# Performance work log

Measured on AMD Instinct MI355X. Metric: run time of the kernel, lower is better.

The kernel has to match this reference:

```python
import jax, jax.numpy as jnp
import numpy as np

LENS = 0.4
DECAY = 0.2
THRESH = 0.2
LOG_SIG_MIN, LOG_SIG_MAX = -20.0, 2.0

# Surrogate-gradient spike: forward is heaviside, backward is rectangular window |x|<lens
@jax.custom_vjp
def act_fun(x):
    return (x > 0.0).astype(x.dtype)

def _act_fwd(x):
    return act_fun(x), x

def _act_bwd(x, g):
    return (g * (jnp.abs(x) < LENS).astype(g.dtype),)

act_fun.defvjp(_act_fwd, _act_bwd)


def _xavier(k, shape):
    fan_out, fan_in = shape
    lim = float(np.sqrt(6.0 / (fan_in + fan_out)))
    return jax.random.uniform(k, shape, jnp.float32, -lim, lim)


def setup_inputs() -> dict:
    key = jax.random.key(0)
    ks = jax.random.split(key, 9)
    B, IN, H, A = 4096, 512, 2048, 32
    return {
        "state": jax.random.normal(ks[0], (B, 5, IN), jnp.float32),
        "W_lif": _xavier(ks[1], (H, IN)), "b_lif": jnp.zeros((H,), jnp.float32),
        "W11": _xavier(ks[2], (H, H)), "b11": jnp.zeros((H,), jnp.float32),
        "W12": _xavier(ks[3], (H, H)), "b12": jnp.zeros((H,), jnp.float32),
        "W21": _xavier(ks[4], (H, H)), "b21": jnp.zeros((H,), jnp.float32),
        "W22": _xavier(ks[5], (H, H)), "b22": jnp.zeros((H,), jnp.float32),
        "Wm": _xavier(ks[6], (A, H)), "bm": jnp.zeros((A,), jnp.float32),
        "Wls": _xavier(ks[7], (A, H)), "bls": jnp.zeros((A,), jnp.float32),
    }


def reference(state, W_lif, b_lif, W11, b11, W12, b12, W21, b21, W22, b22, Wm, bm, Wls, bls):
    x_seq = jnp.repeat(state, 3, axis=1)
    # precompute fc(x) for all steps in one GEMM: [B,15,H]
    fc = jnp.einsum('bti,hi->bth', x_seq, W_lif) + b_lif
    B, T, H = fc.shape

    def step(carry, fc_t):
        mem, spike = carry
        mem1 = mem * DECAY * (1.0 - spike) + fc_t
        spike1 = act_fun(mem1 - THRESH)
        return (mem1, spike1), spike1

    init = (jnp.zeros((B, H), fc.dtype), jnp.zeros((B, H), fc.dtype))
    _, spikes = jax.lax.scan(step, init, jnp.swapaxes(fc, 0, 1))  # [T,B,H]
    x = jnp.mean(spikes, axis=0)  # [B,H]

    x1 = jax.nn.relu(x @ W11.T + b11)
    x1 = jax.nn.relu(x1 @ W12.T + b12)
    mean = x1 @ Wm.T + bm

    x2 = jax.nn.relu(x @ W21.T + b21)
    x2 = jax.nn.relu(x2 @ W22.T + b22)
    log_std = jnp.clip(x2 @ Wls.T + bls, LOG_SIG_MIN, LOG_SIG_MAX)
    return mean, log_std
```

## Files before the change

### kernel.cpp

```cpp
#include <hip/hip_runtime.h>
#include <hip/hip_bf16.h>


typedef _Float16 f16;
using f32x4 = __attribute__((ext_vector_type(4))) float;
using f16x8 = __attribute__((ext_vector_type(8))) f16;

#define MFMA16(a, b, c) __builtin_amdgcn_mfma_f32_16x16x32_f16((a), (b), (c), 0, 0, 0)
#define VMW8()  asm volatile("s_waitcnt vmcnt(8)" ::: "memory")
#define VMW6()  asm volatile("s_waitcnt vmcnt(6)" ::: "memory")
#define VMW0()  asm volatile("s_waitcnt vmcnt(0)" ::: "memory")
#define LGKM0() asm volatile("s_waitcnt lgkmcnt(0)" ::: "memory")
#define BARRIER() __builtin_amdgcn_s_barrier()
#define SCHED0() __builtin_amdgcn_sched_barrier(0)

__device__ __forceinline__ void gload16(const void* g, void* l) {
  __builtin_amdgcn_global_load_lds(
      (const __attribute__((address_space(1))) unsigned int*)g,
      (__attribute__((address_space(3))) unsigned int*)l, 16, 0, 0);
}

__device__ __forceinline__ void cvt8(const float4& a, const float4& b, f16* dst) {
  f16x8 d;
  d[0] = (f16)a.x; d[1] = (f16)a.y; d[2] = (f16)a.z; d[3] = (f16)a.w;
  d[4] = (f16)b.x; d[5] = (f16)b.y; d[6] = (f16)b.z; d[7] = (f16)b.w;
  *(f16x8*)dst = d;
}

__global__ __launch_bounds__(256) void cvtall_kernel(
    const float* __restrict__ state, const float* __restrict__ wlif,
    const float* __restrict__ w11, const float* __restrict__ w21,
    const float* __restrict__ w12, const float* __restrict__ w22,
    const float* __restrict__ wm, const float* __restrict__ wls,
    f16* __restrict__ s16, f16* __restrict__ wl16, f16* __restrict__ w4,
    f16* __restrict__ wmh, f16* __restrict__ wlsh)
{
  int i = blockIdx.x * 256 + threadIdx.x;
  const float* src; f16* dst; int k, ks;
  if (i < 1310720)        { src = state; dst = s16;  k = i;           ks = k; }
  else if (i < 1441792)   { src = wlif;  dst = wl16; k = i - 1310720; ks = k; }
  else if (i < 3538944) {
    int j = i - 1441792; int w = j >> 19;
    src = (w == 0) ? w11 : (w == 1) ? w21 : (w == 2) ? w12 : w22;
    dst = w4; k = j; ks = j & 524287;
  }
  else if (i < 3547136)   { src = wm;  dst = wmh;  k = i - 3538944; ks = k; }
  else if (i < 3555328)   { src = wls; dst = wlsh; k = i - 3547136; ks = k; }
  else return;
  const float4* s4 = (const float4*)src;
  float4 a = s4[(size_t)ks * 2], b = s4[(size_t)ks * 2 + 1];
  cvt8(a, b, dst + (size_t)k * 8);
}

__global__ __launch_bounds__(512, 1) void lif256_kernel(
    const f16* __restrict__ S,
    const f16* __restrict__ W,
    const float* __restrict__ bl,
    f16* __restrict__ X)
{
  __shared__ alignas(16) f16 lds[73728];

  const int tid = threadIdx.x, wid = tid >> 6, lane = tid & 63;
  const int wg = ((int)blockIdx.x % 8) * 32 + (int)blockIdx.x / 8;
  const int bn = wg & 15, bm = wg >> 4;
  const int b0 = bm * 256, h0 = bn * 128;
  const int wr0 = (wid >> 1) * 64, wc0 = (wid & 1) * 64;
  const int fr = lane & 15, fq = lane >> 4;
  const int sr = tid >> 3, scb = (tid & 7) * 16;

  f32x4 acc[4][4] = {};
  float mem[4][4][4] = {};
  unsigned pcnt[4][4] = {};

  char* Lb = (char*)&lds[0];
  const int xsw = (fr & 7) << 4;
  const int x0 = (fq * 16) ^ xsw;
  const int x1 = (64 + fq * 16) ^ xsw;
  char* const pA0 = Lb + (wr0 + fr) * 128 + x0;
  char* const pA1 = Lb + (wr0 + fr) * 128 + x1;
  char* const pB0 = Lb + 98304 + (wc0 + fr) * 128 + x0;
  char* const pB1 = Lb + 98304 + (wc0 + fr) * 128 + x1;

  const f16* sBase[4]; const f16* wBase[2];
#pragma unroll
  for (int l = 0; l < 4; ++l) {
    const int row = l * 64 + sr;
    const int c2 = scb ^ ((row & 7) << 4);
    sBase[l] = S + (size_t)(b0 + row) * 2560 + (c2 >> 1);
  }
#pragma unroll
  for (int l = 0; l < 2; ++l) {
    const int row = l * 64 + sr;
    const int c2 = scb ^ ((row & 7) << 4);
    wBase[l] = W + (size_t)(h0 + row) * 512 + (c2 >> 1);
  }

  auto STAGE = [&](int soA, int soB, int g) {
    const int koff = (g >> 3) * 512 + (g & 7) * 64;
    const int kw = (g & 7) * 64;
#pragma unroll
    for (int l = 0; l < 4; ++l)
      gload16(sBase[l] + koff, Lb + soA + l * 8192 + tid * 16);
#pragma unroll
    for (int l = 0; l < 2; ++l)
      gload16(wBase[l] + kw, Lb + 98304 + soB + l * 8192 + tid * 16);
  };

  const float bias[4] = { bl[h0 + wc0 + fr],      bl[h0 + wc0 + 16 + fr],
                          bl[h0 + wc0 + 32 + fr], bl[h0 + wc0 + 48 + fr] };

  STAGE(0, 0, 0);
  STAGE(32768, 16384, 1);
  VMW6();
  BARRIER();
  SCHED0();

  int soA = 0, soB = 0;
  int soStA = 65536, soStB = 32768;
  for (int g = 0; g < 40; ++g) {
    if (g + 2 < 40) STAGE(soStA, soStB, g + 2);
    SCHED0();

    f16x8 b[4][2], a[4][2];
#pragma unroll
    for (int nf = 0; nf < 4; ++nf) {
      b[nf][0] = *(const f16x8*)(pB0 + soB + nf * 2048);
      b[nf][1] = *(const f16x8*)(pB1 + soB + nf * 2048);
    }
#pragma unroll
    for (int mf = 0; mf < 4; ++mf) {
      a[mf][0] = *(const f16x8*)(pA0 + soA + mf * 2048);
      a[mf][1] = *(const f16x8*)(pA1 + soA + mf * 2048);
    }

    __builtin_amdgcn_s_setprio(1);
#pragma unroll
    for (int mf = 0; mf < 4; ++mf)
#pragma unroll
      for (int nf = 0; nf < 4; ++nf) {
        acc[mf][nf] = MFMA16(a[mf][0], b[nf][0], acc[mf][nf]);
        acc[mf][nf] = MFMA16(a[mf][1], b[nf][1], acc[mf][nf]);
      }
    __builtin_amdgcn_s_setprio(0);

    if ((g & 7) == 7) {
#pragma unroll
      for (int mf = 0; mf < 4; ++mf)
#pragma unroll
        for (int nf = 0; nf < 4; ++nf) {
          unsigned pc = pcnt[mf][nf];
#pragma unroll
          for (int r = 0; r < 4; ++r) {
            const float fc = acc[mf][nf][r] + bias[nf];
            float m = mem[mf][nf][r];
            const unsigned inc = 1u << (8 * r);
#pragma unroll
            for (int j = 0; j < 3; ++j) {
              m = ((m > 0.2f) ? 0.f : m * 0.2f) + fc;
              pc += (m > 0.2f) ? inc : 0u;
            }
            mem[mf][nf][r] = m;
          }
          pcnt[mf][nf] = pc;
          acc[mf][nf] = f32x4{0.f, 0.f, 0.f, 0.f};
        }
    }

    LGKM0();
    if (g + 2 < 40)      { VMW6(); }
    else if (g + 1 < 40) { VMW0(); }
    BARRIER();
    SCHED0();

    soA   = (soA   == 65536) ? 0 : soA   + 32768;
    soB   = (soB   == 32768) ? 0 : soB   + 16384;
    soStA = (soStA == 65536) ? 0 : soStA + 32768;
    soStB = (soStB == 32768) ? 0 : soStB + 16384;
  }

#pragma unroll
  for (int nf = 0; nf < 4; ++nf) {
    const int col = h0 + wc0 + nf * 16 + fr;
#pragma unroll
    for (int mf = 0; mf < 4; ++mf) {
      const int row0 = b0 + wr0 + mf * 16 + fq * 4;
#pragma unroll
      for (int r = 0; r < 4; ++r) {
        const float c = (float)((pcnt[mf][nf] >> (8 * r)) & 255u);
        X[(size_t)(row0 + r) * 2048 + col] = (f16)(c / 15.0f);
      }
    }
  }
}

__global__ __launch_bounds__(512, 2) void trunk256_kernel(
    const f16* __restrict__ A0, const f16* __restrict__ A1, int lda,
    const f16* __restrict__ W0, const f16* __restrict__ W1,
    const float* __restrict__ bb0, const float* __restrict__ bb1,
    f16* __restrict__ C0, f16* __restrict__ C1, int ldc,
    int nbm, int nbn_half, int K)
{
  __shared__ alignas(16) f16 lds[4][256 * 64];

  const int tid = threadIdx.x, wid = tid >> 6, lane = tid & 63;
  const int nwg = nbm * nbn_half * 2, q8 = nwg / 8;
  const int wg = ((int)blockIdx.x % 8) * q8 + (int)blockIdx.x / 8;
  const int bmi = wg % nbm, t = wg / nbm;
  const int half = (t >= nbn_half);
  const f16* Ap = half ? A1 : A0;
  const f16* Wp = half ? W1 : W0;
  const float* bias = half ? bb1 : bb0;
  f16* C = half ? C1 : C0;
  const int bm0 = bmi * 256;
  const int bn0 = (half ? t - nbn_half : t) * 256;

  const int wr0 = (wid >> 2) * 128, wc0 = (wid & 3) * 64;
  const int fr = lane & 15, fq = lane >> 4;
  const int sr = tid >> 3, scb = (tid & 7) * 16;

  f32x4 acc[8][4] = {};
  const int NT = K / 64;

  char* Lb = (char*)&lds[0][0];
  const int xsw = (fr & 7) << 4;
  const int x0 = (fq * 16) ^ xsw;
  const int x1 = (64 + fq * 16) ^ xsw;
  char* const pA0 = Lb + (wr0 + fr) * 128 + x0;
  char* const pA1 = Lb + (wr0 + fr) * 128 + x1;
  char* const pB0 = Lb + 65536 + (wc0 + fr) * 128 + x0;
  char* const pB1 = Lb + 65536 + (wc0 + fr) * 128 + x1;

  const f16* aBase[4]; const f16* wBase[4];
#pragma unroll
  for (int l = 0; l < 4; ++l) {
    const int row = l * 64 + sr;
    const int c2 = scb ^ ((row & 7) << 4);
    aBase[l] = Ap + (size_t)(bm0 + row) * lda + (c2 >> 1);
    wBase[l] = Wp + (size_t)(bn0 + row) * K + (c2 >> 1);
  }

  auto STAGE_A = [&](int slot, int kt) {
    const int koff = kt * 64;
#pragma unroll
    for (int l = 0; l < 4; ++l)
      gload16(aBase[l] + koff, Lb + slot * 32768 + l * 8192 + tid * 16);
  };
  auto STAGE_B = [&](int slot, int kt) {
    const int koff = kt * 64;
#pragma unroll
    for (int l = 0; l < 4; ++l)
      gload16(wBase[l] + koff, Lb + 65536 + slot * 32768 + l * 8192 + tid * 16);
  };

  STAGE_A(0, 0); STAGE_B(0, 0);
  STAGE_A(1, 1); STAGE_B(1, 1);
  VMW8();
  BARRIER();
  SCHED0();

#pragma unroll 2
  for (int kt = 0; kt < NT; ++kt) {
    const int slot = kt & 1;
    const int so = slot * 32768;

    auto QUAD = [&](int mbase, f16x8 (&b)[4][2], f16x8 (&a)[2][2]) {
      __builtin_amdgcn_s_setprio(1);
#pragma unroll
      for (int nf = 0; nf < 4; ++nf) {
        acc[mbase][nf]     = MFMA16(a[0][0], b[nf][0], acc[mbase][nf]);
        acc[mbase][nf]     = MFMA16(a[0][1], b[nf][1], acc[mbase][nf]);
        acc[mbase + 1][nf] = MFMA16(a[1][0], b[nf][0], acc[mbase + 1][nf]);
        acc[mbase + 1][nf] = MFMA16(a[1][1], b[nf][1], acc[mbase + 1][nf]);
      }
      __builtin_amdgcn_s_setprio(0);
    };

    f16x8 b[4][2], a0[2][2], a1[2][2];
#pragma unroll
    for (int nf = 0; nf < 4; ++nf) {
      b[nf][0] = *(const f16x8*)(pB0 + so + nf * 2048);
      b[nf][1] = *(const f16x8*)(pB1 + so + nf * 2048);
    }
#pragma unroll
    for (int i = 0; i < 2; ++i) {
      a0[i][0] = *(const f16x8*)(pA0 + so + i * 2048);
      a0[i][1] = *(const f16x8*)(pA1 + so + i * 2048);
    }
    LGKM0();
    BARRIER();
    if (kt + 2 < NT) STAGE_B(slot, kt + 2);
    SCHED0();

#pragma unroll
    for (int i = 0; i < 2; ++i) {
      a1[i][0] = *(const f16x8*)(pA0 + so + (2 + i) * 2048);
      a1[i][1] = *(const f16x8*)(pA1 + so + (2 + i) * 2048);
    }
    QUAD(0, b, a0);
    LGKM0(); SCHED0();
#pragma unroll
    for (int i = 0; i < 2; ++i) {
      a0[i][0] = *(const f16x8*)(pA0 + so + (4 + i) * 2048);
      a0[i][1] = *(const f16x8*)(pA1 + so + (4 + i) * 2048);
    }
    QUAD(2, b, a1);
    LGKM0(); SCHED0();
#pragma unroll
    for (int i = 0; i < 2; ++i) {
      a1[i][0] = *(const f16x8*)(pA0 + so + (6 + i) * 2048);
      a1[i][1] = *(const f16x8*)(pA1 + so + (6 + i) * 2048);
    }
    QUAD(4, b, a0);
    LGKM0();
    BARRIER();
    if (kt + 2 < NT) STAGE_A(slot, kt + 2);
    SCHED0();
    QUAD(6, b, a1);
    if (kt + 2 < NT)      { VMW8(); }
    else if (kt + 1 < NT) { VMW0(); }
    BARRIER();
    SCHED0();
  }

#pragma unroll
  for (int nf = 0; nf < 4; ++nf) {
    const int col = bn0 + wc0 + nf * 16 + fr;
    const float bv = bias[col];
#pragma unroll
    for (int m = 0; m < 8; ++m) {
      const int row0 = bm0 + wr0 + m * 16 + fq * 4;
#pragma unroll
      for (int r = 0; r < 4; ++r) {
        float v = fmaxf(acc[m][nf][r] + bv, 0.f);
        C[(size_t)(row0 + r) * ldc + col] = (f16)v;
      }
    }
  }
}

__global__ __launch_bounds__(256) void head_kernel(
    const f16* __restrict__ H1, const f16* __restrict__ H2,
    const f16* __restrict__ Wm, const float* __restrict__ bm,
    const f16* __restrict__ Wls, const float* __restrict__ bls,
    float* __restrict__ OUT, int M, int K)
{
  const int tid = threadIdx.x, wid = tid >> 6, lane = tid & 63;
  const int m0 = blockIdx.x * 64 + wid * 16;
  const int kb = (lane >> 4) * 8, fr = lane & 15, fq = lane >> 4;

  f32x4 a1[2] = {}, a2[2] = {};
  for (int k0 = 0; k0 < K; k0 += 32) {
    f16x8 f1 = *(const f16x8*)&H1[(size_t)(m0 + fr) * K + k0 + kb];
    f16x8 f2 = *(const f16x8*)&H2[(size_t)(m0 + fr) * K + k0 + kb];
#pragma unroll
    for (int n = 0; n < 2; ++n) {
      f16x8 wm = *(const f16x8*)&Wm[(size_t)(n * 16 + fr) * K + k0 + kb];
      f16x8 wl = *(const f16x8*)&Wls[(size_t)(n * 16 + fr) * K + k0 + kb];
      a1[n] = MFMA16(f1, wm, a1[n]);
      a2[n] = MFMA16(f2, wl, a2[n]);
    }
  }

#pragma unroll
  for (int n = 0; n < 2; ++n) {
    const int col = n * 16 + fr;
    const float bvm = bm[col];
    const float bvl = bls[col];
#pragma unroll
    for (int r = 0; r < 4; ++r) {
      const int row = m0 + fq * 4 + r;
      OUT[(size_t)row * 32 + col] = a1[n][r] + bvm;
      float lv = a2[n][r] + bvl;
      OUT[(size_t)M * 32 + (size_t)row * 32 + col] = fminf(fmaxf(lv, -20.f), 2.f);
    }
  }
}

extern "C" void kernel_launch(void* const* d_in, const int* in_sizes, int n_in,
                              void* d_out, int out_size, void* d_ws, size_t ws_size,
                              hipStream_t stream) {
  const float* state = (const float*)d_in[0];
  const float* W_lif = (const float*)d_in[1];
  const float* b_lif = (const float*)d_in[2];
  const float* W11   = (const float*)d_in[3];
  const float* b11   = (const float*)d_in[4];
  const float* W12   = (const float*)d_in[5];
  const float* b12   = (const float*)d_in[6];
  const float* W21   = (const float*)d_in[7];
  const float* b21   = (const float*)d_in[8];
  const float* W22   = (const float*)d_in[9];
  const float* b22   = (const float*)d_in[10];
  const float* Wm    = (const float*)d_in[11];
  const float* bm    = (const float*)d_in[12];
  const float* Wls   = (const float*)d_in[13];
  const float* bls   = (const float*)d_in[14];
  float* out = (float*)d_out;

  const int B = 4096, H = 2048;
  char* ws = (char*)d_ws;
  f16* x    = (f16*)(ws);
  f16* s16  = (f16*)(ws + 16777216);
  f16* h1   = (f16*)(ws + 16777216);
  f16* h2   = (f16*)(ws + 33554432);
  f16* wl16 = (f16*)(ws + 37748736);
  f16* w4   = (f16*)(ws + 50331648);
  f16* w11h = (f16*)(ws + 50331648);
  f16* w21h = (f16*)(ws + 58720256);
  f16* h22  = (f16*)(ws + 50331648);
  f16* w12h = (f16*)(ws + 67108864);
  f16* w22h = (f16*)(ws + 75497472);
  f16* wmh  = (f16*)(ws + 83886080);
  f16* wlsh = (f16*)(ws + 84017152);
  f16* h12  = x;

  cvtall_kernel<<<13888, 256, 0, stream>>>(
      state, W_lif, W11, W21, W12, W22, Wm, Wls,
      s16, wl16, w4, wmh, wlsh);

  lif256_kernel<<<256, 512, 0, stream>>>(s16, wl16, b_lif, x);

  trunk256_kernel<<<256, 512, 0, stream>>>(x, x, H, w11h, w21h, b11, b21,
                                           h1, h2, H, 16, 8, H);
  trunk256_kernel<<<256, 512, 0, stream>>>(h1, h2, H, w12h, w22h, b12, b22,
                                           h12, h22, H, 16, 8, H);

  head_kernel<<<B / 64, 256, 0, stream>>>(h12, h22, wmh, bm, wlsh, bls, out, B, H);
}
```

Baseline: 257.5 us.

## Restructure GEMM main loop into finer-grained half-tile staged prefetch pipeline

Rewrites the 256x256 GEMM k-loop as an explicit two-iteration body with a hardcoded trip count of 16 (K=2048). Global-to-LDS loads are split into half-tile chunks and interleaved between each MFMA quad, with the waits adjusted to vmcnt(4). The aim is to spread memory traffic more evenly across compute and shorten the stalls at the end of each iteration. In exchange there are many more barriers per k-step, and the kernel now assumes K=2048, which would break for the K=512 layer if this kernel serves it.

```diff
diff --git a/kernel.cpp b/kernel.cpp
--- a/kernel.cpp
+++ b/kernel.cpp
@@ -7,8 +7,8 @@
 using f16x8 = __attribute__((ext_vector_type(8))) f16;
 
 #define MFMA16(a, b, c) __builtin_amdgcn_mfma_f32_16x16x32_f16((a), (b), (c), 0, 0, 0)
-#define VMW8()  asm volatile("s_waitcnt vmcnt(8)" ::: "memory")
 #define VMW6()  asm volatile("s_waitcnt vmcnt(6)" ::: "memory")
+#define VMW4()  asm volatile("s_waitcnt vmcnt(4)" ::: "memory")
 #define VMW0()  asm volatile("s_waitcnt vmcnt(0)" ::: "memory")
 #define LGKM0() asm volatile("s_waitcnt lgkmcnt(0)" ::: "memory")
 #define BARRIER() __builtin_amdgcn_s_barrier()
@@ -219,7 +219,6 @@
   const int sr = tid >> 3, scb = (tid & 7) * 16;
 
   f32x4 acc[8][4] = {};
-  const int NT = K / 64;
 
   char* Lb = (char*)&lds[0][0];
   const int xsw = (fr & 7) << 4;
@@ -239,87 +238,128 @@
     wBase[l] = Wp + (size_t)(bn0 + row) * K + (c2 >> 1);
   }
 
-  auto STAGE_A = [&](int slot, int kt) {
+  auto STG_A = [&](int bufoff, int h, int kt) {
     const int koff = kt * 64;
 #pragma unroll
-    for (int l = 0; l < 4; ++l)
-      gload16(aBase[l] + koff, Lb + slot * 32768 + l * 8192 + tid * 16);
+    for (int l = 2 * h; l < 2 * h + 2; ++l)
+      gload16(aBase[l] + koff, Lb + bufoff + l * 8192 + tid * 16);
   };
-  auto STAGE_B = [&](int slot, int kt) {
+  auto STG_B = [&](int bufoff, int h, int kt) {
     const int koff = kt * 64;
 #pragma unroll
-    for (int l = 0; l < 4; ++l)
-      gload16(wBase[l] + koff, Lb + 65536 + slot * 32768 + l * 8192 + tid * 16);
+    for (int l = 2 * h; l < 2 * h + 2; ++l)
+      gload16(wBase[l] + koff, Lb + 65536 + bufoff + l * 8192 + tid * 16);
   };
 
-  STAGE_A(0, 0); STAGE_B(0, 0);
-  STAGE_A(1, 1); STAGE_B(1, 1);
-  VMW8();
+  auto QUAD = [&](int mbase, f16x8 (&b)[4][2], f16x8 (&a)[2][2]) {
+    __builtin_amdgcn_s_setprio(1);
+#pragma unroll
+    for (int nf = 0; nf < 4; ++nf) {
+      acc[mbase][nf]     = MFMA16(a[0][0], b[nf][0], acc[mbase][nf]);
+      acc[mbase][nf]     = MFMA16(a[0][1], b[nf][1], acc[mbase][nf]);
+      acc[mbase + 1][nf] = MFMA16(a[1][0], b[nf][0], acc[mbase + 1][nf]);
+      acc[mbase + 1][nf] = MFMA16(a[1][1], b[nf][1], acc[mbase + 1][nf]);
+    }
+    __builtin_amdgcn_s_setprio(0);
+  };
+
+  STG_B(0, 0, 0); STG_B(0, 1, 0);
+  STG_A(0, 0, 0); STG_A(0, 1, 0);
+  STG_B(32768, 0, 1); STG_B(32768, 1, 1);
+  VMW0();
   BARRIER();
   SCHED0();
 
-#pragma unroll 2
-  for (int kt = 0; kt < NT; ++kt) {
-    const int slot = kt & 1;
-    const int so = slot * 32768;
-
-    auto QUAD = [&](int mbase, f16x8 (&b)[4][2], f16x8 (&a)[2][2]) {
-      __builtin_amdgcn_s_setprio(1);
-#pragma unroll
-      for (int nf = 0; nf < 4; ++nf) {
-        acc[mbase][nf]     = MFMA16(a[0][0], b[nf][0], acc[mbase][nf]);
-        acc[mbase][nf]     = MFMA16(a[0][1], b[nf][1], acc[mbase][nf]);
-        acc[mbase + 1][nf] = MFMA16(a[1][0], b[nf][0], acc[mbase + 1][nf]);
-        acc[mbase + 1][nf] = MFMA16(a[1][1], b[nf][1], acc[mbase + 1][nf]);
-      }
-      __builtin_amdgcn_s_setprio(0);
-    };
-
-    f16x8 b[4][2], a0[2][2], a1[2][2];
+  f16x8 b[4][2], a[2][2];
+  for (int i = 0; i < 16; ++i) {
+    const int t1 = 2 * i + 1, u = 2 * i + 2, v = 2 * i + 3;
+    const bool su = (u < 32), sv = (v < 32);
+
 #pragma unroll
     for (int nf = 0; nf < 4; ++nf) {
-      b[nf][0] = *(const f16x8*)(pB0 + so + nf * 2048);
-      b[nf][1] = *(const f16x8*)(pB1 + so + nf * 2048);
-    }
-#pragma unroll
-    for (int i = 0; i < 2; ++i) {
-      a0[i][0] = *(const f16x8*)(pA0 + so + i * 2048);
-      a0[i][1] = *(const f16x8*)(pA1 + so + i * 2048);
-    }
+      b[nf][0] = *(const f16x8*)(pB0 + nf * 2048);
+      b[nf][1] = *(const f16x8*)(pB1 + nf * 2048);
+    }
+#pragma unroll
+    for (int j = 0; j < 2; ++j) {
+      a[j][0] = *(const f16x8*)(pA0 + j * 2048);
+      a[j][1] = *(const f16x8*)(pA1 + j * 2048);
+    }
+    STG_A(32768, 0, t1);
+    LGKM0(); BARRIER(); SCHED0();
+    QUAD(0, b, a);
+
+#pragma unroll
+    for (int j = 0; j < 2; ++j) {
+      a[j][0] = *(const f16x8*)(pA0 + (2 + j) * 2048);
+      a[j][1] = *(const f16x8*)(pA1 + (2 + j) * 2048);
+    }
+    STG_A(32768, 1, t1);
+    LGKM0(); BARRIER(); SCHED0();
+    QUAD(2, b, a);
+
+#pragma unroll
+    for (int j = 0; j < 2; ++j) {
+      a[j][0] = *(const f16x8*)(pA0 + (4 + j) * 2048);
+      a[j][1] = *(const f16x8*)(pA1 + (4 + j) * 2048);
+    }
+    if (su) STG_B(0, 0, u);
+    LGKM0(); BARRIER(); SCHED0();
+    QUAD(4, b, a);
+
+#pragma unroll
+    for (int j = 0; j < 2; ++j) {
+      a[j][0] = *(const f16x8*)(pA0 + (6 + j) * 2048);
+      a[j][1] = *(const f16x8*)(pA1 + (6 + j) * 2048);
+    }
+    if (su) STG_B(0, 1, u);
     LGKM0();
-    BARRIER();
-    if (kt + 2 < NT) STAGE_B(slot, kt + 2);
-    SCHED0();
-
-#pragma unroll
-    for (int i = 0; i < 2; ++i) {
-      a1[i][0] = *(const f16x8*)(pA0 + so + (2 + i) * 2048);
-      a1[i][1] = *(const f16x8*)(pA1 + so + (2 + i) * 2048);
-    }
-    QUAD(0, b, a0);
-    LGKM0(); SCHED0();
-#pragma unroll
-    for (int i = 0; i < 2; ++i) {
-      a0[i][0] = *(const f16x8*)(pA0 + so + (4 + i) * 2048);
-      a0[i][1] = *(const f16x8*)(pA1 + so + (4 + i) * 2048);
-    }
-    QUAD(2, b, a1);
-    LGKM0(); SCHED0();
-#pragma unroll
-    for (int i = 0; i < 2; ++i) {
-      a1[i][0] = *(const f16x8*)(pA0 + so + (6 + i) * 2048);
-      a1[i][1] = *(const f16x8*)(pA1 + so + (6 + i) * 2048);
-    }
-    QUAD(4, b, a0);
+    if (su) { VMW4(); } else { VMW0(); }
+    BARRIER(); SCHED0();
+    QUAD(6, b, a);
+
+#pragma unroll
+    for (int nf = 0; nf < 4; ++nf) {
+      b[nf][0] = *(const f16x8*)(pB0 + 32768 + nf * 2048);
+      b[nf][1] = *(const f16x8*)(pB1 + 32768 + nf * 2048);
+    }
+#pragma unroll
+    for (int j = 0; j < 2; ++j) {
+      a[j][0] = *(const f16x8*)(pA0 + 32768 + j * 2048);
+      a[j][1] = *(const f16x8*)(pA1 + 32768 + j * 2048);
+    }
+    if (su) STG_A(0, 0, u);
+    LGKM0(); BARRIER(); SCHED0();
+    QUAD(0, b, a);
+
+#pragma unroll
+    for (int j = 0; j < 2; ++j) {
+      a[j][0] = *(const f16x8*)(pA0 + 32768 + (2 + j) * 2048);
+      a[j][1] = *(const f16x8*)(pA1 + 32768 + (2 + j) * 2048);
+    }
+    if (su) STG_A(0, 1, u);
+    LGKM0(); BARRIER(); SCHED0();
+    QUAD(2, b, a);
+
+#pragma unroll
+    for (int j = 0; j < 2; ++j) {
+      a[j][0] = *(const f16x8*)(pA0 + 32768 + (4 + j) * 2048);
+      a[j][1] = *(const f16x8*)(pA1 + 32768 + (4 + j) * 2048);
+    }
+    if (sv) STG_B(32768, 0, v);
+    LGKM0(); BARRIER(); SCHED0();
+    QUAD(4, b, a);
+
+#pragma unroll
+    for (int j = 0; j < 2; ++j) {
+      a[j][0] = *(const f16x8*)(pA0 + 32768 + (6 + j) * 2048);
+      a[j][1] = *(const f16x8*)(pA1 + 32768 + (6 + j) * 2048);
+    }
+    if (sv) STG_B(32768, 1, v);
     LGKM0();
-    BARRIER();
-    if (kt + 2 < NT) STAGE_A(slot, kt + 2);
-    SCHED0();
-    QUAD(6, b, a1);
-    if (kt + 2 < NT)      { VMW8(); }
-    else if (kt + 1 < NT) { VMW0(); }
-    BARRIER();
-    SCHED0();
+    if (sv) { VMW4(); } else { VMW0(); }
+    BARRIER(); SCHED0();
+    QUAD(6, b, a);
   }
 
 #pragma unroll
```

Result: no change. 255.8 us (-0.7%).
